# Kernel tuning notes

Hardware: AMD Instinct MI355X
Metric: run time of the kernel (lower is better)

The kernel has to match this reference:

```python
import jax, jax.numpy as jnp
import numpy as np

N, M, D = 32768, 4096, 256   # tokens, codebook_size, dim_feature
COMMITMENT_WEIGHT = 0.25


def setup_inputs() -> dict:
    key = jax.random.key(0)
    kx, ke = jax.random.split(key)
    x = jax.random.normal(kx, (N, D), dtype=jnp.float32)
    # learnable codebook (kaiming-uniform in torch; normal is fine for a numeric baseline)
    embed = jax.random.normal(ke, (M, D), dtype=jnp.float32) * (D ** -0.5)
    return {"x": x, "embed": embed}


def reference(x, embed):
    # argmin over squared distances == argmin over sqrt distances (monotone),
    # matching l2_dist(...).argmin(dim=1) in the original KeOps path.
    x2 = jnp.sum(x * x, axis=-1, keepdims=True)          # [N,1]
    e2 = jnp.sum(embed * embed, axis=-1)                 # [M]
    d2 = x2 - 2.0 * (x @ embed.T) + e2[None, :]          # [N,M]
    idx = jnp.argmin(d2, axis=1)                         # [N] code assignment

    q = embed[idx]                                       # codebook gather [N,D]

    # straight-through estimator: forward value is q, gradient flows to x
    quantized = x + jax.lax.stop_gradient(q - x)

    # commitment loss beta*||sg(x_q) - x||^2 + codebook loss ||x_q - sg(x)||^2
    commit_loss = COMMITMENT_WEIGHT * jnp.mean((jax.lax.stop_gradient(q) - x) ** 2)
    codebook_loss = jnp.mean((q - jax.lax.stop_gradient(x)) ** 2)
    loss = commit_loss + codebook_loss

    # cluster sizes via scatter-add (bincount) and perplexity
    counts = jnp.zeros((M,), jnp.float32).at[idx].add(1.0)
    probs = counts / counts.sum()
    perplexity = jnp.exp(-jnp.sum(probs * jnp.log(probs + 1e-10)))

    return quantized, idx, loss, perplexity
```

## Files before the change

kernel.cpp:

```cpp
#include <hip/hip_runtime.h>
#include <hip/hip_bf16.h>
#include <math.h>

#define NTOK 32768
#define MCB  4096
#define DDIM 256
#define NGATHER 8192

typedef __attribute__((ext_vector_type(8))) short bf16x8;
typedef __attribute__((ext_vector_type(4))) float f32x4;

__device__ __forceinline__ unsigned short f2bf_rne(float f) {
  unsigned int u = __float_as_uint(f);
  unsigned int r = u + 0x7FFFu + ((u >> 16) & 1u);
  return (unsigned short)(r >> 16);
}

__device__ __forceinline__ float bf2f(unsigned short h) {
  return __uint_as_float(((unsigned int)h) << 16);
}

__device__ __forceinline__ void cvt8(const float* f, bf16x8& hi, bf16x8& lo) {
  #pragma unroll
  for (int j = 0; j < 8; ++j) {
    unsigned short hs = f2bf_rne(f[j]);
    float lf = f[j] - bf2f(hs);
    hi[j] = (short)hs;
    lo[j] = (short)f2bf_rne(lf);
  }
}

__device__ __forceinline__ void load_lds16(const void* g, void* l) {
  __builtin_amdgcn_global_load_lds(
      (const __attribute__((address_space(1))) void*)g,
      (__attribute__((address_space(3))) void*)l, 16, 0, 0);
}

__global__ __launch_bounds__(256) void vq_prep_kernel(
    const float* __restrict__ embed, char* __restrict__ ehi,
    char* __restrict__ elo, float* __restrict__ e2) {
  const int id = blockIdx.x * 256 + threadIdx.x;
  const int row = id >> 5;
  const int c = id & 31;
  const float* ep = embed + (size_t)row * DDIM + c * 8;
  const float4 f0 = *(const float4*)(ep);
  const float4 f1 = *(const float4*)(ep + 4);
  float f[8] = {f0.x, f0.y, f0.z, f0.w, f1.x, f1.y, f1.z, f1.w};
  bf16x8 h, l;
  cvt8(f, h, l);
  const size_t off = (size_t)row * 512 + (size_t)(((c ^ (row & 7)) * 16));
  *(bf16x8*)(ehi + off) = h;
  *(bf16x8*)(elo + off) = l;
  float s = 0.0f;
  #pragma unroll
  for (int j = 0; j < 8; ++j) s += f[j] * f[j];
  #pragma unroll
  for (int m = 1; m < 32; m <<= 1) s += __shfl_xor(s, m, 64);
  if (c == 0) e2[row] = s;
}

__global__ __launch_bounds__(256, 2) void vq_main_kernel(
    const float* __restrict__ x, const char* __restrict__ ehi,
    const char* __restrict__ elo, const float* __restrict__ e2,
    float* __restrict__ ws_score, int* __restrict__ ws_idx) {
  __shared__ char lds[65536];
  const int tid = threadIdx.x;
  const int lane = tid & 63;
  const int wv = tid >> 6;
  const int split = blockIdx.x;
  const int row0 = blockIdx.y * 128 + wv * 32;
  const int colbase = split * 1024;
  const int l15 = lane & 15;
  const int l4 = lane >> 4;

  bf16x8 axh[2][8], axl[2][8];
  #pragma unroll
  for (int rf = 0; rf < 2; ++rf) {
    const float* xp = x + (size_t)(row0 + rf * 16 + l15) * DDIM + l4 * 8;
    #pragma unroll
    for (int ks = 0; ks < 8; ++ks) {
      float4 f0 = *(const float4*)(xp + ks * 32);
      float4 f1 = *(const float4*)(xp + ks * 32 + 4);
      float f[8] = {f0.x, f0.y, f0.z, f0.w, f1.x, f1.y, f1.z, f1.w};
      cvt8(f, axh[rf][ks], axl[rf][ks]);
    }
  }

  float minv[2][4];
  int mini[2][4];
  #pragma unroll
  for (int rf = 0; rf < 2; ++rf)
    #pragma unroll
    for (int r = 0; r < 4; ++r) { minv[rf][r] = 3.0e38f; mini[rf][r] = 0; }

  auto stage = [&](int ct, int c) {
    const size_t tb = (size_t)(colbase + ct * 32) * 512 + (size_t)tid * 16;
    const char* ghi = ehi + tb;
    const char* glo = elo + tb;
    char* dst = lds + c * 32768 + tid * 16;
    #pragma unroll
    for (int i = 0; i < 4; ++i) {
      load_lds16(ghi + i * 4096, dst + i * 4096);
      load_lds16(glo + i * 4096, dst + 16384 + i * 4096);
    }
  };

  stage(0, 0);
  __syncthreads();

  for (int ct = 0; ct < 32; ++ct) {
    const int cur = ct & 1;
    if (ct < 31) stage(ct + 1, cur ^ 1);

    const char* base = lds + cur * 32768;
    f32x4 acc[2][2];
    #pragma unroll
    for (int rf = 0; rf < 2; ++rf)
      #pragma unroll
      for (int cf = 0; cf < 2; ++cf) {
        f32x4 z = {0.0f, 0.0f, 0.0f, 0.0f};
        acc[rf][cf] = z;
      }

    #pragma unroll
    for (int ks = 0; ks < 8; ++ks) {
      bf16x8 bh[2], bl[2];
      #pragma unroll
      for (int cf = 0; cf < 2; ++cf) {
        const int brow = cf * 16 + l15;
        const int off = brow * 512 + (((ks * 4 + l4) ^ (brow & 7)) * 16);
        bh[cf] = *(const bf16x8*)(base + off);
        bl[cf] = *(const bf16x8*)(base + 16384 + off);
      }
      #pragma unroll
      for (int rf = 0; rf < 2; ++rf)
        #pragma unroll
        for (int cf = 0; cf < 2; ++cf) {
          f32x4 a = acc[rf][cf];
          a = __builtin_amdgcn_mfma_f32_16x16x32_bf16(axh[rf][ks], bh[cf], a, 0, 0, 0);
          a = __builtin_amdgcn_mfma_f32_16x16x32_bf16(axh[rf][ks], bl[cf], a, 0, 0, 0);
          a = __builtin_amdgcn_mfma_f32_16x16x32_bf16(axl[rf][ks], bh[cf], a, 0, 0, 0);
          acc[rf][cf] = a;
        }
    }

    #pragma unroll
    for (int cf = 0; cf < 2; ++cf) {
      const int col = colbase + ct * 32 + cf * 16 + l15;
      const float ee = e2[col];
      #pragma unroll
      for (int rf = 0; rf < 2; ++rf)
        #pragma unroll
        for (int r = 0; r < 4; ++r) {
          const float s = ee - 2.0f * acc[rf][cf][r];
          if (s < minv[rf][r]) { minv[rf][r] = s; mini[rf][r] = col; }
        }
    }

    __syncthreads();
  }

  #pragma unroll
  for (int rf = 0; rf < 2; ++rf)
    #pragma unroll
    for (int r = 0; r < 4; ++r) {
      float s = minv[rf][r];
      int c = mini[rf][r];
      #pragma unroll
      for (int m = 1; m < 16; m <<= 1) {
        const float os = __shfl_xor(s, m, 64);
        const int oc = __shfl_xor(c, m, 64);
        if (os < s || (os == s && oc < c)) { s = os; c = oc; }
      }
      if (l15 == 0) {
        const int row = row0 + rf * 16 + l4 * 4 + r;
        ws_score[row * 4 + split] = s;
        ws_idx[row * 4 + split] = c;
      }
    }
}

__global__ void vq_merge_kernel(const float* __restrict__ ws_score,
                                const int* __restrict__ ws_idx,
                                int* __restrict__ minidx,
                                float* __restrict__ counts,
                                float* __restrict__ out_idx) {
  const int row = blockIdx.x * 256 + threadIdx.x;
  float bs = ws_score[row * 4];
  int bc = ws_idx[row * 4];
  #pragma unroll
  for (int s2 = 1; s2 < 4; ++s2) {
    const float s = ws_score[row * 4 + s2];
    const int c = ws_idx[row * 4 + s2];
    if (s < bs || (s == bs && c < bc)) { bs = s; bc = c; }
  }
  minidx[row] = bc;
  out_idx[row] = (float)bc;
  atomicAdd(&counts[bc], 1.0f);
}

__global__ __launch_bounds__(256) void vq_gather_kernel(
    const float* __restrict__ x, const float* __restrict__ embed,
    const int* __restrict__ minidx, float* __restrict__ outq,
    double* __restrict__ partials) {
  __shared__ double sh[4];
  const int lane = threadIdx.x & 63;
  const int wv = threadIdx.x >> 6;
  const int row = blockIdx.x * 4 + wv;
  const int idx = minidx[row];
  const float4 q4 = *(const float4*)(embed + (size_t)idx * DDIM + lane * 4);
  const float4 x4 = *(const float4*)(x + (size_t)row * DDIM + lane * 4);
  const float dx = q4.x - x4.x, dy = q4.y - x4.y, dz = q4.z - x4.z, dw = q4.w - x4.w;
  float4 o;
  o.x = x4.x + dx; o.y = x4.y + dy; o.z = x4.z + dz; o.w = x4.w + dw;
  *(float4*)(outq + (size_t)row * DDIM + lane * 4) = o;
  double ss = (double)(dx * dx) + (double)(dy * dy) + (double)(dz * dz) + (double)(dw * dw);
  #pragma unroll
  for (int m = 1; m < 64; m <<= 1) ss += __shfl_xor(ss, m, 64);
  if (lane == 0) sh[wv] = ss;
  __syncthreads();
  if (threadIdx.x == 0) partials[blockIdx.x] = sh[0] + sh[1] + sh[2] + sh[3];
}

__global__ void vq_fin_kernel(const float* __restrict__ counts,
                              const double* __restrict__ partials,
                              float* __restrict__ out) {
  __shared__ double sh[256];
  __shared__ double sl[256];
  double h = 0.0;
  for (int i = threadIdx.x; i < MCB; i += 256) {
    const float p = counts[i] * (1.0f / 32768.0f);
    h += (double)(p * logf(p + 1e-10f));
  }
  double ls = 0.0;
  for (int i = threadIdx.x; i < NGATHER; i += 256) ls += partials[i];
  sh[threadIdx.x] = h;
  sl[threadIdx.x] = ls;
  __syncthreads();
  for (int s = 128; s > 0; s >>= 1) {
    if (threadIdx.x < s) {
      sh[threadIdx.x] += sh[threadIdx.x + s];
      sl[threadIdx.x] += sl[threadIdx.x + s];
    }
    __syncthreads();
  }
  if (threadIdx.x == 0) {
    const size_t base = (size_t)NTOK * DDIM + NTOK;
    out[base] = (float)(1.25 * sl[0] / (double)((size_t)NTOK * DDIM));
    out[base + 1] = (float)exp(-sh[0]);
  }
}

extern "C" void kernel_launch(void* const* d_in, const int* in_sizes, int n_in,
                              void* d_out, int out_size, void* d_ws, size_t ws_size,
                              hipStream_t stream) {
  const float* x = (const float*)d_in[0];
  const float* embed = (const float*)d_in[1];
  float* out = (float*)d_out;
  char* ws = (char*)d_ws;

  float* ws_score = (float*)(ws);
  int* ws_idx = (int*)(ws + 0x80000);
  int* minidx = (int*)(ws + 0x100000);
  float* counts = (float*)(ws + 0x120000);
  double* partials = (double*)(ws + 0x128000);
  float* e2 = (float*)(ws + 0x138000);
  char* ehi = ws + 0x140000;
  char* elo = ws + 0x340000;

  hipMemsetAsync(ws + 0x120000, 0, 16384, stream);
  hipLaunchKernelGGL(vq_prep_kernel, dim3(512), dim3(256), 0, stream,
                     embed, ehi, elo, e2);
  hipLaunchKernelGGL(vq_main_kernel, dim3(4, 256), dim3(256), 0, stream,
                     x, ehi, elo, e2, ws_score, ws_idx);
  hipLaunchKernelGGL(vq_merge_kernel, dim3(128), dim3(256), 0, stream,
                     ws_score, ws_idx, minidx, counts, out + (size_t)NTOK * DDIM);
  hipLaunchKernelGGL(vq_gather_kernel, dim3(NGATHER), dim3(256), 0, stream,
                     x, embed, minidx, out, partials);
  hipLaunchKernelGGL(vq_fin_kernel, dim3(1), dim3(256), 0, stream,
                     counts, partials, out);
}
```

Measured before the change: 266.8 us.

## Restructure VQ distance loop into unrolled double-buffer pipeline with explicit waitcnt

Unrolls the codebook tile loop by two so LDS buffer offsets become compile-time immediates, and precomputes swizzled LDS read pointers instead of recomputing XOR offsets each step. Prefetch of tile t+2 is issued after the compute of tile t, with explicit vmcnt waits and split barriers in place of a single __syncthreads. It also caches e2 in shared memory and raises wave priority around the MFMA block. The aim is to cut address arithmetic, global e2 loads and barrier stalls. In exchange the synchronisation becomes hand-managed and fragile, and the e2s staging store has no barrier of its own before first use.

```diff
diff --git a/kernel.cpp b/kernel.cpp
--- a/kernel.cpp
+++ b/kernel.cpp
@@ -9,6 +9,8 @@
 
 typedef __attribute__((ext_vector_type(8))) short bf16x8;
 typedef __attribute__((ext_vector_type(4))) float f32x4;
+
+template<int V> struct ic { static constexpr int v = V; };
 
 __device__ __forceinline__ unsigned short f2bf_rne(float f) {
   unsigned int u = __float_as_uint(f);
@@ -64,6 +66,7 @@
     const char* __restrict__ elo, const float* __restrict__ e2,
     float* __restrict__ ws_score, int* __restrict__ ws_idx) {
   __shared__ char lds[65536];
+  __shared__ float e2s[1024];
   const int tid = threadIdx.x;
   const int lane = tid & 63;
   const int wv = tid >> 6;
@@ -86,6 +89,8 @@
     }
   }
 
+  *(float4*)&e2s[tid * 4] = *(const float4*)&e2[colbase + tid * 4];
+
   float minv[2][4];
   int mini[2][4];
   #pragma unroll
@@ -93,26 +98,31 @@
     #pragma unroll
     for (int r = 0; r < 4; ++r) { minv[rf][r] = 3.0e38f; mini[rf][r] = 0; }
 
+  const int r3 = l15 & 3;
+  const int b = (l15 >> 2) & 1;
+  const int Veven = l15 * 512 + (l4 ^ r3) * 16 + b * 64;
+  const char* pe = &lds[Veven];
+  const char* po = &lds[Veven + 64 - b * 128];
+
+  const char* gh = ehi + (size_t)colbase * 512 + tid * 16;
+  const char* gl = elo + (size_t)colbase * 512 + tid * 16;
+  char* dst0 = &lds[tid * 16];
+
   auto stage = [&](int ct, int c) {
-    const size_t tb = (size_t)(colbase + ct * 32) * 512 + (size_t)tid * 16;
-    const char* ghi = ehi + tb;
-    const char* glo = elo + tb;
-    char* dst = lds + c * 32768 + tid * 16;
+    const char* sh_ = gh + ct * 16384;
+    const char* sl_ = gl + ct * 16384;
+    char* d = dst0 + c * 32768;
     #pragma unroll
     for (int i = 0; i < 4; ++i) {
-      load_lds16(ghi + i * 4096, dst + i * 4096);
-      load_lds16(glo + i * 4096, dst + 16384 + i * 4096);
+      load_lds16(sh_ + i * 4096, d + i * 4096);
+      load_lds16(sl_ + i * 4096, d + 16384 + i * 4096);
     }
   };
 
-  stage(0, 0);
-  __syncthreads();
-
-  for (int ct = 0; ct < 32; ++ct) {
-    const int cur = ct & 1;
-    if (ct < 31) stage(ct + 1, cur ^ 1);
-
-    const char* base = lds + cur * 32768;
+  auto body = [&](auto pc, int t) {
+    constexpr int P = decltype(pc)::v * 32768;
+    const float ee0 = e2s[t * 32 + l15];
+    const float ee1 = e2s[t * 32 + 16 + l15];
     f32x4 acc[2][2];
     #pragma unroll
     for (int rf = 0; rf < 2; ++rf)
@@ -121,43 +131,73 @@
         f32x4 z = {0.0f, 0.0f, 0.0f, 0.0f};
         acc[rf][cf] = z;
       }
-
+    __builtin_amdgcn_s_setprio(1);
     #pragma unroll
     for (int ks = 0; ks < 8; ++ks) {
-      bf16x8 bh[2], bl[2];
+      const char* pb = (ks & 1) ? po : pe;
+      const int kimm = P + (ks >> 1) * 128;
+      bf16x8 bh0 = *(const bf16x8*)(pb + kimm);
+      bf16x8 bh1 = *(const bf16x8*)(pb + kimm + 8192);
+      bf16x8 bl0 = *(const bf16x8*)(pb + kimm + 16384);
+      bf16x8 bl1 = *(const bf16x8*)(pb + kimm + 24576);
       #pragma unroll
-      for (int cf = 0; cf < 2; ++cf) {
-        const int brow = cf * 16 + l15;
-        const int off = brow * 512 + (((ks * 4 + l4) ^ (brow & 7)) * 16);
-        bh[cf] = *(const bf16x8*)(base + off);
-        bl[cf] = *(const bf16x8*)(base + 16384 + off);
-      }
-      #pragma unroll
-      for (int rf = 0; rf < 2; ++rf)
-        #pragma unroll
-        for (int cf = 0; cf < 2; ++cf) {
-          f32x4 a = acc[rf][cf];
-          a = __builtin_amdgcn_mfma_f32_16x16x32_bf16(axh[rf][ks], bh[cf], a, 0, 0, 0);
-          a = __builtin_amdgcn_mfma_f32_16x16x32_bf16(axh[rf][ks], bl[cf], a, 0, 0, 0);
-          a = __builtin_amdgcn_mfma_f32_16x16x32_bf16(axl[rf][ks], bh[cf], a, 0, 0, 0);
-          acc[rf][cf] = a;
-        }
-    }
-
+      for (int rf = 0; rf < 2; ++rf) {
+        f32x4 a0 = acc[rf][0];
+        a0 = __builtin_amdgcn_mfma_f32_16x16x32_bf16(axh[rf][ks], bh0, a0, 0, 0, 0);
+        a0 = __builtin_amdgcn_mfma_f32_16x16x32_bf16(axh[rf][ks], bl0, a0, 0, 0, 0);
+        a0 = __builtin_amdgcn_mfma_f32_16x16x32_bf16(axl[rf][ks], bh0, a0, 0, 0, 0);
+        acc[rf][0] = a0;
+        f32x4 a1 = acc[rf][1];
+        a1 = __builtin_amdgcn_mfma_f32_16x16x32_bf16(axh[rf][ks], bh1, a1, 0, 0, 0);
+        a1 = __builtin_amdgcn_mfma_f32_16x16x32_bf16(axh[rf][ks], bl1, a1, 0, 0, 0);
+        a1 = __builtin_amdgcn_mfma_f32_16x16x32_bf16(axl[rf][ks], bh1, a1, 0, 0, 0);
+        acc[rf][1] = a1;
+      }
+    }
+    __builtin_amdgcn_s_setprio(0);
     #pragma unroll
     for (int cf = 0; cf < 2; ++cf) {
-      const int col = colbase + ct * 32 + cf * 16 + l15;
-      const float ee = e2[col];
+      const int col = colbase + t * 32 + cf * 16 + l15;
+      const float ee = cf ? ee1 : ee0;
       #pragma unroll
       for (int rf = 0; rf < 2; ++rf)
         #pragma unroll
         for (int r = 0; r < 4; ++r) {
-          const float s = ee - 2.0f * acc[rf][cf][r];
+          const float s = fmaf(-2.0f, acc[rf][cf][r], ee);
           if (s < minv[rf][r]) { minv[rf][r] = s; mini[rf][r] = col; }
         }
     }
-
-    __syncthreads();
+  };
+
+  stage(0, 0);
+  __syncthreads();
+  stage(1, 1);
+
+  for (int t = 0; t < 32; t += 2) {
+    body(ic<0>{}, t);
+    __builtin_amdgcn_s_barrier();
+    if (t < 30) {
+      stage(t + 2, 0);
+      asm volatile("s_waitcnt vmcnt(8)" ::: "memory");
+    } else {
+      asm volatile("s_waitcnt vmcnt(0)" ::: "memory");
+    }
+    __builtin_amdgcn_sched_barrier(0);
+    __builtin_amdgcn_s_barrier();
+    __builtin_amdgcn_sched_barrier(0);
+    body(ic<1>{}, t + 1);
+    if (t < 30) {
+      __builtin_amdgcn_s_barrier();
+      if (t < 29) {
+        stage(t + 3, 1);
+        asm volatile("s_waitcnt vmcnt(8)" ::: "memory");
+      } else {
+        asm volatile("s_waitcnt vmcnt(0)" ::: "memory");
+      }
+      __builtin_amdgcn_sched_barrier(0);
+      __builtin_amdgcn_s_barrier();
+      __builtin_amdgcn_sched_barrier(0);
+    }
   }
 
   #pragma unroll
```

Result: slower. 275.2 us (+3.1%).
